# Performance work log

Hardware: AMD Instinct MI355X
Metric: run time of the kernel (lower is better)

The kernel has to match this reference:

```python
import jax, jax.numpy as jnp
import numpy as np

SCORE_THRESHOLD = 0.5
IOU_THRESHOLD = 0.5


def _pairwise_iou(boxes):
    # boxes: [N, 4] in xyxy
    x1, y1, x2, y2 = boxes[:, 0], boxes[:, 1], boxes[:, 2], boxes[:, 3]
    area = (x2 - x1) * (y2 - y1)  # [N]
    ix1 = jnp.maximum(x1[:, None], x1[None, :])
    iy1 = jnp.maximum(y1[:, None], y1[None, :])
    ix2 = jnp.minimum(x2[:, None], x2[None, :])
    iy2 = jnp.minimum(y2[:, None], y2[None, :])
    iw = jnp.clip(ix2 - ix1, 0.0)
    ih = jnp.clip(iy2 - iy1, 0.0)
    inter = iw * ih  # [N, N]
    union = area[:, None] + area[None, :] - inter
    return inter / jnp.maximum(union, 1e-9)


def setup_inputs() -> dict:
    key = jax.random.key(0)
    rtdetr_raw_out = jax.random.uniform(key, (1, 8192, 5), dtype=jnp.float32)
    return {"rtdetr_raw_out": rtdetr_raw_out}


def reference(rtdetr_raw_out):
    x = rtdetr_raw_out[0]                      # [N, 5]
    cxcywh = x[:, :4]
    conf = x[:, 4]
    conf = conf / jnp.max(conf)                # normalize by max score
    cx, cy, w, h = cxcywh[:, 0], cxcywh[:, 1], cxcywh[:, 2], cxcywh[:, 3]
    xyxy = jnp.stack([cx - w * 0.5, cy - h * 0.5, cx + w * 0.5, cy + h * 0.5], axis=1)
    valid = conf >= SCORE_THRESHOLD            # score filter
    N = xyxy.shape[0]
    # sort by descending score (torchvision nms processes boxes in score order)
    order = jnp.argsort(-conf)
    boxes_s = xyxy[order]
    scores_s = conf[order]
    valid_s = valid[order]
    iou = _pairwise_iou(boxes_s)               # [N, N]
    idx = jnp.arange(N)

    def body(i, keep):
        # if box i survives, suppress all lower-score boxes with IoU > thr
        sup = keep[i] & (iou[i] > IOU_THRESHOLD) & (idx > i)
        return keep & ~sup

    keep = jax.lax.fori_loop(0, N, body, valid_s)
    out = jnp.concatenate([boxes_s, scores_s[:, None]], axis=1)  # [N, 5]
    # fixed-shape output: suppressed / below-threshold rows are zeroed
    return jnp.where(keep[:, None], out, 0.0)
```

## Files before the change

### kernel.cpp

```cpp
#include <hip/hip_runtime.h>
#include <cstdint>

typedef unsigned long long ull;

#define N_BOX 8192
#define CH 512
#define WPC 8
#define NCH 16

#define OFF_TB     0
#define OFF_TC     3440640
#define OFF_TD     3932160
#define OFF_BOXES  4456448
#define OFF_SCORES 4587520
#define OFF_CTRL   4620288
#define OFF_KEPT   4689920
#define OFF_PUSH   4691968

#define CTRL_VB    512
#define PFLAG      1024
#define KSTRIDE    16

#define A_LD(p)    __hip_atomic_load((p), __ATOMIC_RELAXED, __HIP_MEMORY_SCOPE_AGENT)
#define A_ST(p,v)  __hip_atomic_store((p), (v), __ATOMIC_RELAXED, __HIP_MEMORY_SCOPE_AGENT)
#define A_STR(p,v) __hip_atomic_store((p), (v), __ATOMIC_RELEASE, __HIP_MEMORY_SCOPE_AGENT)

__device__ __forceinline__ int rows_before2(int c) {
    return 7424 * c - 256 * c * c;
}

__device__ __forceinline__ ull make_key(float s, int idx) {
    return (((ull)__float_as_uint(s)) << 13) | (ull)(8191 - idx);
}

__device__ __forceinline__ float box_area(float4 b) {
    return __fmul_rn(__fsub_rn(b.z, b.x), __fsub_rn(b.w, b.y));
}

__device__ __forceinline__ bool iou_gt_half(float4 a, float aarea, float4 b, float barea) {
    float ix1 = fmaxf(a.x, b.x);
    float iy1 = fmaxf(a.y, b.y);
    float ix2 = fminf(a.z, b.z);
    float iy2 = fminf(a.w, b.w);
    float iw = fmaxf(__fsub_rn(ix2, ix1), 0.0f);
    float ih = fmaxf(__fsub_rn(iy2, iy1), 0.0f);
    float inter = __fmul_rn(iw, ih);
    float uni = __fsub_rn(__fadd_rn(aarea, barea), inter);
    float iou = __fdiv_rn(inter, fmaxf(uni, 1e-9f));
    return iou > 0.5f;
}

__global__ __launch_bounds__(256) void k123_rank_scatter(const float* __restrict__ in,
                                                         float4* __restrict__ boxes4,
                                                         float* __restrict__ scores,
                                                         int* __restrict__ ctrl) {
    __shared__ ull keys[N_BOX];
    __shared__ float wm[4];
    __shared__ int wv[4];
    int t = threadIdx.x;
    int bx = blockIdx.x;

    float cf[32];
    float m = 0.0f;
    #pragma unroll
    for (int r = 0; r < 32; ++r) {
        cf[r] = in[(r * 256 + t) * 5 + 4];
        m = fmaxf(m, cf[r]);
    }
    for (int off = 32; off; off >>= 1) m = fmaxf(m, __shfl_down(m, off));
    if ((t & 63) == 0) wm[t >> 6] = m;
    __syncthreads();
    float maxc = fmaxf(fmaxf(wm[0], wm[1]), fmaxf(wm[2], wm[3]));

    #pragma unroll
    for (int r = 0; r < 32; ++r) {
        int k = r * 256 + t;
        keys[k] = make_key(__fdiv_rn(cf[r], maxc), k);
    }
    __syncthreads();

    int il = t >> 3, seg = t & 7;
    int i = bx * 32 + il;
    ull ki = keys[i];
    const ull* kb = keys + seg;
    int cnt = 0;
    #pragma unroll 8
    for (int cc = 0; cc < 1024; ++cc)
        cnt += (kb[cc * 8] > ki) ? 1 : 0;
    cnt += __shfl_down(cnt, 4, 8);
    cnt += __shfl_down(cnt, 2, 8);
    cnt += __shfl_down(cnt, 1, 8);

    if (seg == 0) {
        int r = cnt;
        float cx = in[i * 5 + 0];
        float cy = in[i * 5 + 1];
        float w  = in[i * 5 + 2];
        float h  = in[i * 5 + 3];
        float s  = __fdiv_rn(in[i * 5 + 4], maxc);
        float4 b;
        b.x = __fsub_rn(cx, __fmul_rn(w, 0.5f));
        b.y = __fsub_rn(cy, __fmul_rn(h, 0.5f));
        b.z = __fadd_rn(cx, __fmul_rn(w, 0.5f));
        b.w = __fadd_rn(cy, __fmul_rn(h, 0.5f));
        boxes4[r] = b;
        scores[r] = s;
    }

    if (bx == 0) {
        const ull kthr = ((ull)0x3F000000u) << 13;
        int cv = 0;
        for (int k = t; k < N_BOX; k += 256) cv += (keys[k] >= kthr) ? 1 : 0;
        for (int off = 32; off; off >>= 1) cv += __shfl_down(cv, off);
        if ((t & 63) == 0) wv[t >> 6] = cv;
        if (t < NCH) ctrl[t * 32] = 0;
        if (t < NCH) ctrl[PFLAG + t * 32] = 0;
        __syncthreads();
        if (t == 0) ctrl[CTRL_VB] = wv[0] + wv[1] + wv[2] + wv[3];
    }
}

__global__ __launch_bounds__(256) void k4_build(const float4* __restrict__ boxes4,
                                                const float* __restrict__ scores,
                                                ull* __restrict__ TB,
                                                ull* __restrict__ TC,
                                                ull* __restrict__ TD) {
    __shared__ float4 sb[CH];
    __shared__ float sa[CH];
    int bid = blockIdx.x;
    int t = threadIdx.x;
    int c;
    int mode;
    int j0;
    if (bid >= 1920) {
        mode = 2;
        int d = bid - 1920;
        c = d >> 4;
        j0 = (d & 15) * 32;
    } else if (bid >= 1680) {
        mode = 1;
        int d = bid - 1680;
        c = d >> 4;
        j0 = (d & 15) * 32;
    } else {
        mode = 0;
        c = 0;
        int rem = bid;
        while (rem >= 224 - 16 * c) { rem -= 224 - 16 * c; ++c; }
        j0 = CH * (c + 2) + rem * 32;
    }
    if (scores[c * CH] < 0.5f) return;
    if (mode == 0 && scores[j0] < 0.5f) return;

    for (int i = t; i < CH; i += 256) {
        float4 b = boxes4[c * CH + i];
        sb[i] = b;
        sa[i] = box_area(b);
    }
    __syncthreads();

    int w = t & 7;
    int r = t >> 3;
    int jl = j0 + r;
    float4 me;
    float ma;
    int lim = 64;
    if (mode == 2) {
        me = sb[jl];
        ma = sa[jl];
        int wj = jl >> 6;
        lim = (w < wj) ? 64 : ((w == wj) ? (jl & 63) : 0);
    } else if (mode == 1) {
        me = boxes4[CH * (c + 1) + jl];
        ma = box_area(me);
    } else {
        me = boxes4[jl];
        ma = box_area(me);
    }
    ull bits = 0;
    #pragma unroll 8
    for (int k = 0; k < 64; ++k) {
        int kk = (k + w) & 63;
        if (kk < lim &&
            iou_gt_half(sb[w * 64 + kk], sa[w * 64 + kk], me, ma))
            bits |= 1ull << kk;
    }
    if (mode == 2)      TD[c * 4096 + w * 512 + jl] = bits;
    else if (mode == 1) TC[c * 4096 + w * 512 + jl] = bits;
    else TB[(size_t)(rows_before2(c) + (jl - CH * (c + 2))) * WPC + w] = bits;
}

__global__ __launch_bounds__(1024) void k5_nms(const float4* __restrict__ boxes4,
                                               const float* __restrict__ scores,
                                               const ull* __restrict__ TBg,
                                               const ull* __restrict__ TCg,
                                               const ull* __restrict__ TDg,
                                               ull* __restrict__ keptg,
                                               ull* __restrict__ pusha,
                                               int* __restrict__ ctrl,
                                               float* __restrict__ out) {
    __shared__ ull TDs[CH * WPC];
    __shared__ ull TCs[CH * WPC];
    __shared__ ull kwsh[WPC];
    __shared__ ull darr[WPC];
    __shared__ unsigned amask[16];
    int c = blockIdx.x;
    int t = threadIdx.x;
    int lane = t & 63;
    int wave = t >> 6;
    int vb = ctrl[CTRL_VB];
    int nchv = (vb + CH - 1) / CH;

    if (c < nchv) {
        {
            const ulonglong2* src = (const ulonglong2*)(TDg + (size_t)c * CH * WPC);
            ulonglong2* dst = (ulonglong2*)TDs;
            #pragma unroll
            for (int i2 = t; i2 < CH * WPC / 2; i2 += 1024) dst[i2] = src[i2];
        }
        if (c + 1 < nchv) {
            const ulonglong2* src = (const ulonglong2*)(TCg + (size_t)c * CH * WPC);
            ulonglong2* dst = (ulonglong2*)TCs;
            #pragma unroll
            for (int i2 = t; i2 < CH * WPC / 2; i2 += 1024) dst[i2] = src[i2];
        }
        if (t < 16) {
            int n = vb - (c * 16 + t) * 32;
            amask[t] = (n >= 32) ? 0xffffffffu : ((n <= 0) ? 0u : ((1u << n) - 1u));
        }
        __syncthreads();

        for (int cp = 0; cp + 2 <= c; ++cp) {
            if (wave == 0) {
                if (lane == 0) { while (A_LD(&ctrl[cp * 32]) != 1) {} }
                if (lane < WPC) kwsh[lane] = A_LD(&keptg[cp * KSTRIDE + lane]);
            }
            __syncthreads();
            ull anyk = kwsh[0] | kwsh[1] | kwsh[2] | kwsh[3] |
                       kwsh[4] | kwsh[5] | kwsh[6] | kwsh[7];
            if (anyk && t < CH) {
                if ((amask[t >> 5] >> (t & 31)) & 1u) {
                    const ull* row = TBg +
                        (size_t)(rows_before2(cp) + (c * CH + t - CH * (cp + 2))) * WPC;
                    ull a = 0;
                    #pragma unroll
                    for (int q = 0; q < WPC; ++q) a |= row[q] & kwsh[q];
                    if (a) atomicAnd(&amask[t >> 5], ~(1u << (t & 31)));
                }
            }
            __syncthreads();
        }

        if (c > 0) {
            if (wave == 0) {
                if (lane == 0) { while (A_LD(&ctrl[PFLAG + c * 32]) != 1) {} }
                if (lane < WPC) kwsh[lane] = A_LD(&pusha[c * KSTRIDE + lane]);
            }
            __syncthreads();
            if (t < WPC) {
                ull s = kwsh[t];
                amask[2 * t]     &= ~(unsigned)s;
                amask[2 * t + 1] &= ~(unsigned)(s >> 32);
            }
            __syncthreads();
        }

        if (wave == 0) {
            ull alive[WPC];
            #pragma unroll
            for (int w = 0; w < WPC; ++w)
                alive[w] = (ull)amask[2 * w] | ((ull)amask[2 * w + 1] << 32);
            const ull* T = TDs;
            #pragma unroll
            for (int w = 0; w < WPC; ++w) {
                ull word = alive[w];
                if (!word) continue;
                ull Tc[WPC];
                #pragma unroll
                for (int j = 0; j < WPC; ++j)
                    if (j >= w) Tc[j] = T[w * 512 + j * 64 + lane];
                ull td = Tc[w];
                ull a2 = word, kept = 0;
                while (a2 & ~kept) {
                    bool al = (a2 >> lane) & 1;
                    bool kp = (kept >> lane) & 1;
                    ull nk = __ballot(al && !kp && ((td & a2) == 0));
                    ull nd = __ballot(al && !kp && ((td & kept) != 0));
                    kept |= nk;
                    a2 &= ~nd;
                }
                alive[w] = kept;
                #pragma unroll
                for (int j = 0; j < WPC; ++j) {
                    if (j <= w) continue;
                    if (!alive[j]) continue;
                    alive[j] &= ~__ballot((Tc[j] & kept) != 0);
                }
            }
            if (lane == 0) {
                #pragma unroll
                for (int w = 0; w < WPC; ++w) {
                    A_ST(&keptg[c * KSTRIDE + w], alive[w]);
                    amask[2 * w]     = (unsigned)alive[w];
                    amask[2 * w + 1] = (unsigned)(alive[w] >> 32);
                }
                A_STR(&ctrl[c * 32], 1);
            }
        }
        __syncthreads();

        if (c + 1 < nchv) {
            if (wave < WPC) {
                ull kw[WPC];
                #pragma unroll
                for (int w = 0; w < WPC; ++w)
                    kw[w] = (ull)amask[2 * w] | ((ull)amask[2 * w + 1] << 32);
                bool dead = false;
                #pragma unroll
                for (int w = 0; w < WPC; ++w) {
                    if (kw[w]) dead |= (TCs[w * 512 + wave * 64 + lane] & kw[w]) != 0ull;
                }
                ull d = __ballot(dead);
                if (lane == 0) darr[wave] = d;
            }
            __syncthreads();
            if (t == 0) {
                #pragma unroll
                for (int w = 0; w < WPC; ++w)
                    A_ST(&pusha[(c + 1) * KSTRIDE + w], darr[w]);
                A_STR(&ctrl[PFLAG + (c + 1) * 32], 1);
            }
        }
        __syncthreads();
    } else {
        if (t < 16) amask[t] = 0u;
        __syncthreads();
    }

    if (t < CH) {
        int j = c * CH + t;
        bool kept = (amask[t >> 5] >> (t & 31)) & 1u;
        float4 b = boxes4[j];
        float s = scores[j];
        out[j * 5 + 0] = kept ? b.x : 0.0f;
        out[j * 5 + 1] = kept ? b.y : 0.0f;
        out[j * 5 + 2] = kept ? b.z : 0.0f;
        out[j * 5 + 3] = kept ? b.w : 0.0f;
        out[j * 5 + 4] = kept ? s   : 0.0f;
    }
}

extern "C" void kernel_launch(void* const* d_in, const int* in_sizes, int n_in,
                              void* d_out, int out_size, void* d_ws, size_t ws_size,
                              hipStream_t stream) {
    const float* in = (const float*)d_in[0];
    char* ws = (char*)d_ws;
    ull* TB        = (ull*)(ws + OFF_TB);
    ull* TC        = (ull*)(ws + OFF_TC);
    ull* TD        = (ull*)(ws + OFF_TD);
    float4* boxes4 = (float4*)(ws + OFF_BOXES);
    float* scores  = (float*)(ws + OFF_SCORES);
    int* ctrl      = (int*)(ws + OFF_CTRL);
    ull* keptg     = (ull*)(ws + OFF_KEPT);
    ull* pusha     = (ull*)(ws + OFF_PUSH);
    float* out     = (float*)d_out;

    k123_rank_scatter<<<256, 256, 0, stream>>>(in, boxes4, scores, ctrl);
    k4_build<<<2176, 256, 0, stream>>>(boxes4, scores, TB, TC, TD);
    k5_nms<<<NCH, 1024, 0, stream>>>(boxes4, scores, TB, TC, TD, keptg, pusha, ctrl, out);
}
```

Baseline: 121.1 us.

## Pair NMS chunks per block and rank keys from registers instead of shared memory

The rank kernel no longer stages all 8192 sort keys in LDS. Each thread keeps its 32 keys in registers, and the block counts ranks for its 32 boxes through wave reductions and shared atomics. The NMS kernel now runs 8 blocks, each handling two consecutive 512-box chunks. Chunk b is pruned by chunk a locally in shared memory, which removes one cross-block push/flag handshake per pair and lets cross-chunk suppression for both chunks happen in one pass. The trade-off is more serialized work per block, fewer blocks in flight, and more register pressure.

```diff
diff --git a/kernel.cpp b/kernel.cpp
--- a/kernel.cpp
+++ b/kernel.cpp
@@ -50,15 +50,17 @@
     return iou > 0.5f;
 }
 
-__global__ __launch_bounds__(256) void k123_rank_scatter(const float* __restrict__ in,
-                                                         float4* __restrict__ boxes4,
-                                                         float* __restrict__ scores,
-                                                         int* __restrict__ ctrl) {
-    __shared__ ull keys[N_BOX];
+__global__ __launch_bounds__(256) void kA_rank_scatter(const float* __restrict__ in,
+                                                       float4* __restrict__ boxes4,
+                                                       float* __restrict__ scores,
+                                                       int* __restrict__ ctrl) {
+    __shared__ ull ikey[32];
+    __shared__ int rank32[32];
     __shared__ float wm[4];
     __shared__ int wv[4];
     int t = threadIdx.x;
     int bx = blockIdx.x;
+    if (t < 32) rank32[t] = 0;
 
     float cf[32];
     float m = 0.0f;
@@ -72,27 +74,28 @@
     __syncthreads();
     float maxc = fmaxf(fmaxf(wm[0], wm[1]), fmaxf(wm[2], wm[3]));
 
+    ull kk[32];
     #pragma unroll
-    for (int r = 0; r < 32; ++r) {
-        int k = r * 256 + t;
-        keys[k] = make_key(__fdiv_rn(cf[r], maxc), k);
-    }
+    for (int r = 0; r < 32; ++r)
+        kk[r] = make_key(__fdiv_rn(cf[r], maxc), r * 256 + t);
+
+    int il = t - ((bx & 7) * 32);
+    if (il >= 0 && il < 32) ikey[il] = kk[bx >> 3];
     __syncthreads();
 
-    int il = t >> 3, seg = t & 7;
-    int i = bx * 32 + il;
-    ull ki = keys[i];
-    const ull* kb = keys + seg;
-    int cnt = 0;
-    #pragma unroll 8
-    for (int cc = 0; cc < 1024; ++cc)
-        cnt += (kb[cc * 8] > ki) ? 1 : 0;
-    cnt += __shfl_down(cnt, 4, 8);
-    cnt += __shfl_down(cnt, 2, 8);
-    cnt += __shfl_down(cnt, 1, 8);
-
-    if (seg == 0) {
-        int r = cnt;
+    for (int ii = 0; ii < 32; ++ii) {
+        ull ik = ikey[ii];
+        int cnt = 0;
+        #pragma unroll
+        for (int r = 0; r < 32; ++r) cnt += (kk[r] > ik) ? 1 : 0;
+        for (int off = 32; off; off >>= 1) cnt += __shfl_down(cnt, off);
+        if ((t & 63) == 0) atomicAdd(&rank32[ii], cnt);
+    }
+    __syncthreads();
+
+    if (t < 32) {
+        int i = bx * 32 + t;
+        int r = rank32[t];
         float cx = in[i * 5 + 0];
         float cy = in[i * 5 + 1];
         float w  = in[i * 5 + 2];
@@ -110,7 +113,8 @@
     if (bx == 0) {
         const ull kthr = ((ull)0x3F000000u) << 13;
         int cv = 0;
-        for (int k = t; k < N_BOX; k += 256) cv += (keys[k] >= kthr) ? 1 : 0;
+        #pragma unroll
+        for (int r = 0; r < 32; ++r) cv += (kk[r] >= kthr) ? 1 : 0;
         for (int off = 32; off; off >>= 1) cv += __shfl_down(cv, off);
         if ((t & 63) == 0) wv[t >> 6] = cv;
         if (t < NCH) ctrl[t * 32] = 0;
@@ -190,6 +194,49 @@
     else TB[(size_t)(rows_before2(c) + (jl - CH * (c + 2))) * WPC + w] = bits;
 }
 
+__device__ __forceinline__ void scan_chunk(const ull* T, unsigned* am,
+                                           ull* keptrow, int* flag, int lane) {
+    ull alive[WPC];
+    #pragma unroll
+    for (int w = 0; w < WPC; ++w)
+        alive[w] = (ull)am[2 * w] | ((ull)am[2 * w + 1] << 32);
+    #pragma unroll
+    for (int w = 0; w < WPC; ++w) {
+        ull word = alive[w];
+        if (!word) continue;
+        ull Tc[WPC];
+        #pragma unroll
+        for (int j = 0; j < WPC; ++j)
+            if (j >= w) Tc[j] = T[w * 512 + j * 64 + lane];
+        ull td = Tc[w];
+        ull a2 = word, kept = 0;
+        while (a2 & ~kept) {
+            bool al = (a2 >> lane) & 1;
+            bool kp = (kept >> lane) & 1;
+            ull nk = __ballot(al && !kp && ((td & a2) == 0));
+            ull nd = __ballot(al && !kp && ((td & kept) != 0));
+            kept |= nk;
+            a2 &= ~nd;
+        }
+        alive[w] = kept;
+        #pragma unroll
+        for (int j = 0; j < WPC; ++j) {
+            if (j <= w) continue;
+            if (!alive[j]) continue;
+            alive[j] &= ~__ballot((Tc[j] & kept) != 0);
+        }
+    }
+    if (lane == 0) {
+        #pragma unroll
+        for (int w = 0; w < WPC; ++w) {
+            A_ST(&keptrow[w], alive[w]);
+            am[2 * w]     = (unsigned)alive[w];
+            am[2 * w + 1] = (unsigned)(alive[w] >> 32);
+        }
+        A_STR(flag, 1);
+    }
+}
+
 __global__ __launch_bounds__(1024) void k5_nms(const float4* __restrict__ boxes4,
                                                const float* __restrict__ scores,
                                                const ull* __restrict__ TBg,
@@ -199,38 +246,55 @@
                                                ull* __restrict__ pusha,
                                                int* __restrict__ ctrl,
                                                float* __restrict__ out) {
-    __shared__ ull TDs[CH * WPC];
-    __shared__ ull TCs[CH * WPC];
+    __shared__ ull TDs[8192];
     __shared__ ull kwsh[WPC];
     __shared__ ull darr[WPC];
-    __shared__ unsigned amask[16];
-    int c = blockIdx.x;
-    int t = threadIdx.x;
-    int lane = t & 63;
-    int wave = t >> 6;
+    __shared__ unsigned amask[32];
+    const int c = blockIdx.x;
+    const int t = threadIdx.x;
+    const int lane = t & 63;
+    const int wave = t >> 6;
+    const int a = 2 * c;
+    const int b = a + 1;
     int vb = ctrl[CTRL_VB];
     int nchv = (vb + CH - 1) / CH;
-
-    if (c < nchv) {
+    bool aLive = (a < nchv);
+    bool bLive = (b < nchv);
+
+    if (aLive) {
         {
-            const ulonglong2* src = (const ulonglong2*)(TDg + (size_t)c * CH * WPC);
+            const ulonglong2* src = (const ulonglong2*)(TDg + (size_t)a * 4096);
             ulonglong2* dst = (ulonglong2*)TDs;
             #pragma unroll
-            for (int i2 = t; i2 < CH * WPC / 2; i2 += 1024) dst[i2] = src[i2];
-        }
-        if (c + 1 < nchv) {
-            const ulonglong2* src = (const ulonglong2*)(TCg + (size_t)c * CH * WPC);
-            ulonglong2* dst = (ulonglong2*)TCs;
+            for (int i2 = t; i2 < 2048; i2 += 1024) dst[i2] = src[i2];
+        }
+        if (bLive) {
+            const ulonglong2* src = (const ulonglong2*)(TDg + (size_t)b * 4096);
+            ulonglong2* dst = (ulonglong2*)(TDs + 4096);
             #pragma unroll
-            for (int i2 = t; i2 < CH * WPC / 2; i2 += 1024) dst[i2] = src[i2];
-        }
-        if (t < 16) {
-            int n = vb - (c * 16 + t) * 32;
+            for (int i2 = t; i2 < 2048; i2 += 1024) dst[i2] = src[i2];
+        }
+        if (t < 32) {
+            int n = vb - (a * 16 + t) * 32;
             amask[t] = (n >= 32) ? 0xffffffffu : ((n <= 0) ? 0u : ((1u << n) - 1u));
         }
+
+        ull tca[WPC], tcb[WPC];
+        if (bLive && wave < WPC) {
+            const ull* p = TCg + (size_t)a * 4096 + wave * 64 + lane;
+            #pragma unroll
+            for (int w = 0; w < WPC; ++w) tca[w] = p[w * 512];
+        }
+        if (b + 1 < nchv && wave < WPC) {
+            const ull* p = TCg + (size_t)b * 4096 + wave * 64 + lane;
+            #pragma unroll
+            for (int w = 0; w < WPC; ++w) tcb[w] = p[w * 512];
+        }
         __syncthreads();
 
-        for (int cp = 0; cp + 2 <= c; ++cp) {
+        int cpmax = bLive ? (a - 1) : (a - 2);
+        if (cpmax > 13) cpmax = 13;
+        for (int cp = 0; cp <= cpmax; ++cp) {
             if (wave == 0) {
                 if (lane == 0) { while (A_LD(&ctrl[cp * 32]) != 1) {} }
                 if (lane < WPC) kwsh[lane] = A_LD(&keptg[cp * KSTRIDE + lane]);
@@ -238,23 +302,27 @@
             __syncthreads();
             ull anyk = kwsh[0] | kwsh[1] | kwsh[2] | kwsh[3] |
                        kwsh[4] | kwsh[5] | kwsh[6] | kwsh[7];
-            if (anyk && t < CH) {
-                if ((amask[t >> 5] >> (t & 31)) & 1u) {
+            if (anyk) {
+                int jl = t & 511;
+                int ch = (t < 512) ? a : b;
+                bool act = (t < 512) ? (cp <= a - 2) : bLive;
+                if (act && ((amask[t >> 5] >> (t & 31)) & 1u)) {
+                    int j = ch * CH + jl;
                     const ull* row = TBg +
-                        (size_t)(rows_before2(cp) + (c * CH + t - CH * (cp + 2))) * WPC;
-                    ull a = 0;
+                        (size_t)(rows_before2(cp) + (j - CH * (cp + 2))) * WPC;
+                    ull x = 0;
                     #pragma unroll
-                    for (int q = 0; q < WPC; ++q) a |= row[q] & kwsh[q];
-                    if (a) atomicAnd(&amask[t >> 5], ~(1u << (t & 31)));
+                    for (int q = 0; q < WPC; ++q) x |= row[q] & kwsh[q];
+                    if (x) atomicAnd(&amask[t >> 5], ~(1u << (t & 31)));
                 }
             }
             __syncthreads();
         }
 
-        if (c > 0) {
+        if (a > 0) {
             if (wave == 0) {
-                if (lane == 0) { while (A_LD(&ctrl[PFLAG + c * 32]) != 1) {} }
-                if (lane < WPC) kwsh[lane] = A_LD(&pusha[c * KSTRIDE + lane]);
+                if (lane == 0) { while (A_LD(&ctrl[PFLAG + a * 32]) != 1) {} }
+                if (lane < WPC) kwsh[lane] = A_LD(&pusha[a * KSTRIDE + lane]);
             }
             __syncthreads();
             if (t < WPC) {
@@ -265,88 +333,67 @@
             __syncthreads();
         }
 
-        if (wave == 0) {
-            ull alive[WPC];
-            #pragma unroll
-            for (int w = 0; w < WPC; ++w)
-                alive[w] = (ull)amask[2 * w] | ((ull)amask[2 * w + 1] << 32);
-            const ull* T = TDs;
-            #pragma unroll
-            for (int w = 0; w < WPC; ++w) {
-                ull word = alive[w];
-                if (!word) continue;
-                ull Tc[WPC];
-                #pragma unroll
-                for (int j = 0; j < WPC; ++j)
-                    if (j >= w) Tc[j] = T[w * 512 + j * 64 + lane];
-                ull td = Tc[w];
-                ull a2 = word, kept = 0;
-                while (a2 & ~kept) {
-                    bool al = (a2 >> lane) & 1;
-                    bool kp = (kept >> lane) & 1;
-                    ull nk = __ballot(al && !kp && ((td & a2) == 0));
-                    ull nd = __ballot(al && !kp && ((td & kept) != 0));
-                    kept |= nk;
-                    a2 &= ~nd;
-                }
-                alive[w] = kept;
-                #pragma unroll
-                for (int j = 0; j < WPC; ++j) {
-                    if (j <= w) continue;
-                    if (!alive[j]) continue;
-                    alive[j] &= ~__ballot((Tc[j] & kept) != 0);
-                }
-            }
-            if (lane == 0) {
-                #pragma unroll
-                for (int w = 0; w < WPC; ++w) {
-                    A_ST(&keptg[c * KSTRIDE + w], alive[w]);
-                    amask[2 * w]     = (unsigned)alive[w];
-                    amask[2 * w + 1] = (unsigned)(alive[w] >> 32);
-                }
-                A_STR(&ctrl[c * 32], 1);
-            }
-        }
+        if (wave == 0)
+            scan_chunk(TDs, amask, &keptg[a * KSTRIDE], &ctrl[a * 32], lane);
         __syncthreads();
 
-        if (c + 1 < nchv) {
+        if (bLive) {
             if (wave < WPC) {
-                ull kw[WPC];
-                #pragma unroll
-                for (int w = 0; w < WPC; ++w)
-                    kw[w] = (ull)amask[2 * w] | ((ull)amask[2 * w + 1] << 32);
                 bool dead = false;
                 #pragma unroll
                 for (int w = 0; w < WPC; ++w) {
-                    if (kw[w]) dead |= (TCs[w * 512 + wave * 64 + lane] & kw[w]) != 0ull;
+                    ull kw = (ull)amask[2 * w] | ((ull)amask[2 * w + 1] << 32);
+                    if (kw) dead |= (tca[w] & kw) != 0ull;
                 }
                 ull d = __ballot(dead);
-                if (lane == 0) darr[wave] = d;
-            }
-            __syncthreads();
-            if (t == 0) {
-                #pragma unroll
-                for (int w = 0; w < WPC; ++w)
-                    A_ST(&pusha[(c + 1) * KSTRIDE + w], darr[w]);
-                A_STR(&ctrl[PFLAG + (c + 1) * 32], 1);
+                if (lane == 0 && d) {
+                    amask[16 + 2 * wave]     &= ~(unsigned)d;
+                    amask[16 + 2 * wave + 1] &= ~(unsigned)(d >> 32);
+                }
+            }
+            __syncthreads();
+
+            if (wave == 0)
+                scan_chunk(TDs + 4096, amask + 16, &keptg[b * KSTRIDE],
+                           &ctrl[b * 32], lane);
+            __syncthreads();
+
+            if (b + 1 < nchv) {
+                if (wave < WPC) {
+                    bool dead = false;
+                    #pragma unroll
+                    for (int w = 0; w < WPC; ++w) {
+                        ull kw = (ull)amask[16 + 2 * w] | ((ull)amask[16 + 2 * w + 1] << 32);
+                        if (kw) dead |= (tcb[w] & kw) != 0ull;
+                    }
+                    ull d = __ballot(dead);
+                    if (lane == 0) darr[wave] = d;
+                }
+                __syncthreads();
+                if (t == 0) {
+                    #pragma unroll
+                    for (int w = 0; w < WPC; ++w)
+                        A_ST(&pusha[(b + 1) * KSTRIDE + w], darr[w]);
+                    A_STR(&ctrl[PFLAG + (b + 1) * 32], 1);
+                }
             }
         }
         __syncthreads();
     } else {
-        if (t < 16) amask[t] = 0u;
+        if (t < 32) amask[t] = 0u;
         __syncthreads();
     }
 
-    if (t < CH) {
-        int j = c * CH + t;
+    {
+        int j = a * CH + t;
         bool kept = (amask[t >> 5] >> (t & 31)) & 1u;
-        float4 b = boxes4[j];
+        float4 bx = boxes4[j];
         float s = scores[j];
-        out[j * 5 + 0] = kept ? b.x : 0.0f;
-        out[j * 5 + 1] = kept ? b.y : 0.0f;
-        out[j * 5 + 2] = kept ? b.z : 0.0f;
-        out[j * 5 + 3] = kept ? b.w : 0.0f;
-        out[j * 5 + 4] = kept ? s   : 0.0f;
+        out[j * 5 + 0] = kept ? bx.x : 0.0f;
+        out[j * 5 + 1] = kept ? bx.y : 0.0f;
+        out[j * 5 + 2] = kept ? bx.z : 0.0f;
+        out[j * 5 + 3] = kept ? bx.w : 0.0f;
+        out[j * 5 + 4] = kept ? s    : 0.0f;
     }
 }
 
@@ -365,7 +412,7 @@
     ull* pusha     = (ull*)(ws + OFF_PUSH);
     float* out     = (float*)d_out;
 
-    k123_rank_scatter<<<256, 256, 0, stream>>>(in, boxes4, scores, ctrl);
+    kA_rank_scatter<<<256, 256, 0, stream>>>(in, boxes4, scores, ctrl);
     k4_build<<<2176, 256, 0, stream>>>(boxes4, scores, TB, TC, TD);
-    k5_nms<<<NCH, 1024, 0, stream>>>(boxes4, scores, TB, TC, TD, keptg, pusha, ctrl, out);
-}
+    k5_nms<<<8, 1024, 0, stream>>>(boxes4, scores, TB, TC, TD, keptg, pusha, ctrl, out);
+}
```

After: 123.1 us. Within noise of the previous version (+1.6%).

## Resolve intra-word NMS serially via precomputed row-major suppression masks

Applied to the files above, without the earlier changes.

Adds a new mode to the build kernel that computes, for each box, a 64-bit mask of the later boxes it suppresses within its own 64-box word (row-major form). The NMS kernel loads these masks into registers and settles each word with a ctz-driven serial scan plus a shuffle, replacing the iterative ballot fixed-point loop over the transposed diagonal tile. This is meant to cut the number of ballot rounds on the serial critical path. The cost is 32 extra build blocks and one extra global load per lane. The serial loop still runs once per surviving box in each word.

```diff
diff --git a/kernel.cpp b/kernel.cpp
--- a/kernel.cpp
+++ b/kernel.cpp
@@ -16,6 +16,7 @@
 #define OFF_CTRL   4620288
 #define OFF_KEPT   4689920
 #define OFF_PUSH   4691968
+#define OFF_TDC    4694144
 
 #define CTRL_VB    512
 #define PFLAG      1024
@@ -124,7 +125,8 @@
                                                 const float* __restrict__ scores,
                                                 ull* __restrict__ TB,
                                                 ull* __restrict__ TC,
-                                                ull* __restrict__ TD) {
+                                                ull* __restrict__ TD,
+                                                ull* __restrict__ TDC) {
     __shared__ float4 sb[CH];
     __shared__ float sa[CH];
     int bid = blockIdx.x;
@@ -132,7 +134,12 @@
     int c;
     int mode;
     int j0;
-    if (bid >= 1920) {
+    if (bid >= 2176) {
+        mode = 3;
+        int d = bid - 2176;
+        c = d >> 1;
+        j0 = (d & 1) * 256;
+    } else if (bid >= 1920) {
         mode = 2;
         int d = bid - 1920;
         c = d >> 4;
@@ -158,6 +165,23 @@
         sa[i] = box_area(b);
     }
     __syncthreads();
+
+    if (mode == 3) {
+        int s = j0 + t;
+        int w = s >> 6, k = s & 63;
+        float4 me = sb[s];
+        float ma = sa[s];
+        ull bits = 0;
+        #pragma unroll 8
+        for (int mth = 0; mth < 64; ++mth) {
+            int j = (mth + k) & 63;
+            if (j > k &&
+                iou_gt_half(sb[w * 64 + j], sa[w * 64 + j], me, ma))
+                bits |= 1ull << j;
+        }
+        TDC[c * 512 + s] = bits;
+        return;
+    }
 
     int w = t & 7;
     int r = t >> 3;
@@ -195,6 +219,7 @@
                                                const ull* __restrict__ TBg,
                                                const ull* __restrict__ TCg,
                                                const ull* __restrict__ TDg,
+                                               const ull* __restrict__ TDCg,
                                                ull* __restrict__ keptg,
                                                ull* __restrict__ pusha,
                                                int* __restrict__ ctrl,
@@ -212,6 +237,12 @@
     int nchv = (vb + CH - 1) / CH;
 
     if (c < nchv) {
+        ull tdc[WPC];
+        if (wave == 0) {
+            #pragma unroll
+            for (int w = 0; w < WPC; ++w)
+                tdc[w] = TDCg[c * 512 + w * 64 + lane];
+        }
         {
             const ulonglong2* src = (const ulonglong2*)(TDg + (size_t)c * CH * WPC);
             ulonglong2* dst = (ulonglong2*)TDs;
@@ -273,21 +304,19 @@
             const ull* T = TDs;
             #pragma unroll
             for (int w = 0; w < WPC; ++w) {
-                ull word = alive[w];
-                if (!word) continue;
+                ull a2 = alive[w];
+                if (!a2) continue;
                 ull Tc[WPC];
                 #pragma unroll
                 for (int j = 0; j < WPC; ++j)
-                    if (j >= w) Tc[j] = T[w * 512 + j * 64 + lane];
-                ull td = Tc[w];
-                ull a2 = word, kept = 0;
-                while (a2 & ~kept) {
-                    bool al = (a2 >> lane) & 1;
-                    bool kp = (kept >> lane) & 1;
-                    ull nk = __ballot(al && !kp && ((td & a2) == 0));
-                    ull nd = __ballot(al && !kp && ((td & kept) != 0));
-                    kept |= nk;
-                    a2 &= ~nd;
+                    if (j > w) Tc[j] = T[w * 512 + j * 64 + lane];
+                ull kept = 0;
+                while (a2) {
+                    int k = __builtin_ctzll(a2);
+                    kept |= 1ull << k;
+                    ull sc = __shfl(tdc[w], k);
+                    a2 &= ~sc;
+                    a2 &= ~(1ull << k);
                 }
                 alive[w] = kept;
                 #pragma unroll
@@ -363,9 +392,11 @@
     int* ctrl      = (int*)(ws + OFF_CTRL);
     ull* keptg     = (ull*)(ws + OFF_KEPT);
     ull* pusha     = (ull*)(ws + OFF_PUSH);
+    ull* TDC       = (ull*)(ws + OFF_TDC);
     float* out     = (float*)d_out;
 
     k123_rank_scatter<<<256, 256, 0, stream>>>(in, boxes4, scores, ctrl);
-    k4_build<<<2176, 256, 0, stream>>>(boxes4, scores, TB, TC, TD);
-    k5_nms<<<NCH, 1024, 0, stream>>>(boxes4, scores, TB, TC, TD, keptg, pusha, ctrl, out);
-}
+    k4_build<<<2208, 256, 0, stream>>>(boxes4, scores, TB, TC, TD, TDC);
+    k5_nms<<<NCH, 1024, 0, stream>>>(boxes4, scores, TB, TC, TD, TDC,
+                                     keptg, pusha, ctrl, out);
+}
```

Measured after the change: 200.2 us. 65.3% more time.
